# Performance work log

Hardware: AMD Instinct MI355X
Metric: run time of the kernel (lower is better)

The kernel has to match this reference:

```python
import jax, jax.numpy as jnp
import numpy as np

N_NODES = 50000
N_EDGES = 800000
FT = 128
HID = 128
N_EXTRA_LAYERS = 2  # num_layers - 1


def _gin_conv(x, src, dst, W1, b1, W2, b2):
    # GINConv with eps=0: mlp(x + sum_{j->i} x_j)
    agg = jax.ops.segment_sum(x[src], dst, num_segments=N_NODES)
    h = x + agg
    h = jax.nn.relu(h @ W1 + b1)
    return h @ W2 + b2


def setup_inputs() -> dict:
    key = jax.random.key(0)
    ks = jax.random.split(key, 12)
    feat = jax.random.normal(ks[0], (N_NODES, FT), dtype=jnp.float32)
    edge_index = jax.random.randint(ks[1], (2, N_EDGES), 0, N_NODES, dtype=jnp.int32)
    s = 0.02
    # layer 0: ft -> hid
    W1a = jax.random.normal(ks[2], (FT, HID), dtype=jnp.float32) * s
    b1a = jnp.zeros((HID,), dtype=jnp.float32)
    W2a = jax.random.normal(ks[3], (HID, HID), dtype=jnp.float32) * s
    b2a = jnp.zeros((HID,), dtype=jnp.float32)
    # remaining layers stacked: [L, hid, hid]
    Ws1 = jax.random.normal(ks[4], (N_EXTRA_LAYERS, HID, HID), dtype=jnp.float32) * s
    bs1 = jnp.zeros((N_EXTRA_LAYERS, HID), dtype=jnp.float32)
    Ws2 = jax.random.normal(ks[5], (N_EXTRA_LAYERS, HID, HID), dtype=jnp.float32) * s
    bs2 = jnp.zeros((N_EXTRA_LAYERS, HID), dtype=jnp.float32)
    return {"feat": feat, "edge_index": edge_index,
            "W1a": W1a, "b1a": b1a, "W2a": W2a, "b2a": b2a,
            "Ws1": Ws1, "bs1": bs1, "Ws2": Ws2, "bs2": bs2}


def reference(feat, edge_index, W1a, b1a, W2a, b2a, Ws1, bs1, Ws2, bs2):
    src = edge_index[0]
    dst = edge_index[1]
    x = jax.nn.relu(_gin_conv(feat, src, dst, W1a, b1a, W2a, b2a))
    for i in range(N_EXTRA_LAYERS):
        x = jax.nn.relu(_gin_conv(x, src, dst, Ws1[i], bs1[i], Ws2[i], bs2[i]))
    return x[None]  # [1, N, hid]
```

## Files before the change

### kernel.cpp

```cpp
#include <hip/hip_runtime.h>
#include <hip/hip_bf16.h>

#define N_NODES 50000
#define N_EDGES 800000
#define HID 128

typedef __attribute__((ext_vector_type(8))) short bf16x8;
typedef __attribute__((ext_vector_type(4))) float f32x4;

__device__ inline ushort f32_to_bf16_bits(float v) {
    union { float f; unsigned u; } a; a.f = v;
    unsigned r = a.u + 0x7fff + ((a.u >> 16) & 1);
    return (ushort)(r >> 16);
}
__device__ inline float bf16bits_to_f32(ushort b) {
    union { float f; unsigned u; } a; a.u = ((unsigned)b) << 16;
    return a.f;
}


__global__ __launch_bounds__(256) void hist_kernel(const int* __restrict__ dst,
                                                   int* __restrict__ cnt) {
    int e = blockIdx.x * 256 + threadIdx.x;
    if (e < N_EDGES) atomicAdd(&cnt[dst[e]], 1);
}

__global__ __launch_bounds__(256) void alloc_offsets_kernel(const int* __restrict__ cnt,
                                                            int* __restrict__ offs,
                                                            int* __restrict__ cursor,
                                                            int* __restrict__ gcur) {
    int i = blockIdx.x * 256 + threadIdx.x;
    int lane = threadIdx.x & 63;
    int c = (i < N_NODES) ? cnt[i] : 0;
    int pre = c;
    #pragma unroll
    for (int d = 1; d < 64; d <<= 1) {
        int t = __shfl_up(pre, d);
        if (lane >= d) pre += t;
    }
    int base = 0;
    if (lane == 63) base = atomicAdd(gcur, pre);
    base = __shfl(base, 63);
    int o = base + pre - c;
    if (i < N_NODES) { offs[i] = o; cursor[i] = o; }
}

__global__ __launch_bounds__(256) void scatter_kernel(const int* __restrict__ src,
                                                      const int* __restrict__ dst,
                                                      int* __restrict__ cursor,
                                                      int* __restrict__ csr) {
    int e = blockIdx.x * 256 + threadIdx.x;
    if (e < N_EDGES) {
        int d = dst[e];
        int pos = atomicAdd(&cursor[d], 1);
        csr[pos] = src[e];
    }
}


__global__ __launch_bounds__(256) void conv_kernel(const float* __restrict__ in,
                                                   ushort* __restrict__ out) {
    int t = blockIdx.x * 256 + threadIdx.x;
    if (t >= (N_NODES * HID) / 8) return;
    const float4* in4 = (const float4*)in;
    float4 a = in4[2 * t], b = in4[2 * t + 1];
    float v[8] = {a.x, a.y, a.z, a.w, b.x, b.y, b.z, b.w};
    uint4 o;
    o.x = (unsigned)f32_to_bf16_bits(v[0]) | ((unsigned)f32_to_bf16_bits(v[1]) << 16);
    o.y = (unsigned)f32_to_bf16_bits(v[2]) | ((unsigned)f32_to_bf16_bits(v[3]) << 16);
    o.z = (unsigned)f32_to_bf16_bits(v[4]) | ((unsigned)f32_to_bf16_bits(v[5]) << 16);
    o.w = (unsigned)f32_to_bf16_bits(v[6]) | ((unsigned)f32_to_bf16_bits(v[7]) << 16);
    ((uint4*)out)[t] = o;
}


__global__ __launch_bounds__(256) void prep_kernel(const float* __restrict__ W1a,
                                                   const float* __restrict__ W2a,
                                                   const float* __restrict__ Ws1,
                                                   const float* __restrict__ Ws2,
                                                   short* __restrict__ whi,
                                                   short* __restrict__ wlo) {
    int mat = blockIdx.y;
    const float* W;
    switch (mat) {
        case 0: W = W1a; break;
        case 1: W = W2a; break;
        case 2: W = Ws1; break;
        case 3: W = Ws2; break;
        case 4: W = Ws1 + HID * HID; break;
        default: W = Ws2 + HID * HID; break;
    }
    int tid2 = blockIdx.x * 256 + threadIdx.x;
    int l = tid2 & 63;
    int ft = tid2 >> 6;
    int t = ft & 3, f = ft >> 2;
    int g = l >> 4, lm = l & 15;
    bf16x8 hv, lv;
    #pragma unroll
    for (int i = 0; i < 8; ++i) {
        int k = t * 32 + g * 8 + i;
        int n = f * 16 + lm;
        float v = W[k * HID + n];
        ushort hb = f32_to_bf16_bits(v);
        ushort lb = f32_to_bf16_bits(v - bf16bits_to_f32(hb));
        hv[i] = (short)hb;
        lv[i] = (short)lb;
    }
    size_t base = ((size_t)mat * 2048 + tid2) * 8;
    *(bf16x8*)&whi[base] = hv;
    *(bf16x8*)&wlo[base] = lv;
}


__global__ __launch_bounds__(256) void fused_gin_kernel(const unsigned* __restrict__ xbf,
                                                        const int* __restrict__ csr,
                                                        const int* __restrict__ offs,
                                                        const int* __restrict__ cnt,
                                                        const short* __restrict__ w1hi,
                                                        const short* __restrict__ w1lo,
                                                        const short* __restrict__ w2hi,
                                                        const short* __restrict__ w2lo,
                                                        const float* __restrict__ b1,
                                                        const float* __restrict__ b2,
                                                        ushort* __restrict__ xoutb,
                                                        float* __restrict__ xoutf) {
    __shared__ short sHi[16][136];
    __shared__ short sLo[16][136];

    const int tid = threadIdx.x;
    const int lane = tid & 63;
    const int wid = tid >> 6;
    const int nbase = blockIdx.x * 16;
    const int g = lane >> 4, lm = lane & 15;

    for (int n = 0; n < 4; ++n) {
        int node = nbase + wid * 4 + n;
        int off = offs[node];
        int c = cnt[node];
        unsigned su = xbf[(size_t)node * 64 + lane];
        float ax = __uint_as_float(su << 16);
        float ay = __uint_as_float(su & 0xffff0000u);
        int e = 0;
        for (; e + 8 <= c; e += 8) {
            int s[8];
            #pragma unroll
            for (int q = 0; q < 8; ++q) s[q] = csr[off + e + q];
            unsigned u[8];
            #pragma unroll
            for (int q = 0; q < 8; ++q) u[q] = xbf[(size_t)s[q] * 64 + lane];
            #pragma unroll
            for (int q = 0; q < 8; ++q) {
                ax += __uint_as_float(u[q] << 16);
                ay += __uint_as_float(u[q] & 0xffff0000u);
            }
        }
        for (; e + 4 <= c; e += 4) {
            int s0 = csr[off + e], s1 = csr[off + e + 1];
            int s2 = csr[off + e + 2], s3 = csr[off + e + 3];
            unsigned u0 = xbf[(size_t)s0 * 64 + lane];
            unsigned u1 = xbf[(size_t)s1 * 64 + lane];
            unsigned u2 = xbf[(size_t)s2 * 64 + lane];
            unsigned u3 = xbf[(size_t)s3 * 64 + lane];
            ax += (__uint_as_float(u0 << 16) + __uint_as_float(u1 << 16)) +
                  (__uint_as_float(u2 << 16) + __uint_as_float(u3 << 16));
            ay += (__uint_as_float(u0 & 0xffff0000u) + __uint_as_float(u1 & 0xffff0000u)) +
                  (__uint_as_float(u2 & 0xffff0000u) + __uint_as_float(u3 & 0xffff0000u));
        }
        for (; e < c; ++e) {
            int s = csr[off + e];
            unsigned u = xbf[(size_t)s * 64 + lane];
            ax += __uint_as_float(u << 16);
            ay += __uint_as_float(u & 0xffff0000u);
        }
        ushort hx = f32_to_bf16_bits(ax);
        ushort lx = f32_to_bf16_bits(ax - bf16bits_to_f32(hx));
        ushort hy = f32_to_bf16_bits(ay);
        ushort ly = f32_to_bf16_bits(ay - bf16bits_to_f32(hy));
        int row = wid * 4 + n;
        *(unsigned*)&sHi[row][2 * lane] = (unsigned)hx | ((unsigned)hy << 16);
        *(unsigned*)&sLo[row][2 * lane] = (unsigned)lx | ((unsigned)ly << 16);
    }
    __syncthreads();

    f32x4 accT[2];

    {
        bf16x8 ahi[4], alo[4];
        #pragma unroll
        for (int t = 0; t < 4; ++t) {
            ahi[t] = *(bf16x8*)&sHi[lm][t * 32 + g * 8];
            alo[t] = *(bf16x8*)&sLo[lm][t * 32 + g * 8];
        }
        __syncthreads();
        #pragma unroll
        for (int ff = 0; ff < 2; ++ff) {
            int f = wid * 2 + ff;
            const bf16x8* bh = (const bf16x8*)&w1hi[((size_t)(f * 4) * 64 + lane) * 8];
            const bf16x8* bl = (const bf16x8*)&w1lo[((size_t)(f * 4) * 64 + lane) * 8];
            f32x4 acc = {0.f, 0.f, 0.f, 0.f};
            #pragma unroll
            for (int t = 0; t < 4; ++t) {
                bf16x8 bhv = bh[t * 64];
                bf16x8 blv = bl[t * 64];
                acc = __builtin_amdgcn_mfma_f32_16x16x32_bf16(ahi[t], bhv, acc, 0, 0, 0);
                acc = __builtin_amdgcn_mfma_f32_16x16x32_bf16(alo[t], bhv, acc, 0, 0, 0);
                acc = __builtin_amdgcn_mfma_f32_16x16x32_bf16(ahi[t], blv, acc, 0, 0, 0);
            }
            accT[ff] = acc;
        }
    }
    #pragma unroll
    for (int ff = 0; ff < 2; ++ff) {
        int f = wid * 2 + ff;
        float bv = b1[f * 16 + lm];
        #pragma unroll
        for (int r = 0; r < 4; ++r) {
            float v = accT[ff][r] + bv;
            v = v > 0.f ? v : 0.f;
            ushort hb = f32_to_bf16_bits(v);
            ushort lb = f32_to_bf16_bits(v - bf16bits_to_f32(hb));
            int m = g * 4 + r;
            sHi[m][f * 16 + lm] = (short)hb;
            sLo[m][f * 16 + lm] = (short)lb;
        }
    }
    __syncthreads();

    {
        bf16x8 ahi[4], alo[4];
        #pragma unroll
        for (int t = 0; t < 4; ++t) {
            ahi[t] = *(bf16x8*)&sHi[lm][t * 32 + g * 8];
            alo[t] = *(bf16x8*)&sLo[lm][t * 32 + g * 8];
        }
        #pragma unroll
        for (int ff = 0; ff < 2; ++ff) {
            int f = wid * 2 + ff;
            const bf16x8* bh = (const bf16x8*)&w2hi[((size_t)(f * 4) * 64 + lane) * 8];
            const bf16x8* bl = (const bf16x8*)&w2lo[((size_t)(f * 4) * 64 + lane) * 8];
            f32x4 acc = {0.f, 0.f, 0.f, 0.f};
            #pragma unroll
            for (int t = 0; t < 4; ++t) {
                bf16x8 bhv = bh[t * 64];
                bf16x8 blv = bl[t * 64];
                acc = __builtin_amdgcn_mfma_f32_16x16x32_bf16(ahi[t], bhv, acc, 0, 0, 0);
                acc = __builtin_amdgcn_mfma_f32_16x16x32_bf16(alo[t], bhv, acc, 0, 0, 0);
                acc = __builtin_amdgcn_mfma_f32_16x16x32_bf16(ahi[t], blv, acc, 0, 0, 0);
            }
            accT[ff] = acc;
        }
    }
    #pragma unroll
    for (int ff = 0; ff < 2; ++ff) {
        int f = wid * 2 + ff;
        float bv = b2[f * 16 + lm];
        #pragma unroll
        for (int r = 0; r < 4; ++r) {
            float v = accT[ff][r] + bv;
            v = v > 0.f ? v : 0.f;
            int gn = nbase + g * 4 + r;
            size_t gi = (size_t)gn * HID + f * 16 + lm;
            if (xoutb) xoutb[gi] = f32_to_bf16_bits(v);
            if (xoutf) xoutf[gi] = v;
        }
    }
}


extern "C" void kernel_launch(void* const* d_in, const int* in_sizes, int n_in,
                              void* d_out, int out_size, void* d_ws, size_t ws_size,
                              hipStream_t stream) {
    const float* feat = (const float*)d_in[0];
    const int* edge = (const int*)d_in[1];
    const int* src = edge;
    const int* dst = edge + N_EDGES;
    const float* W1a = (const float*)d_in[2];
    const float* b1a = (const float*)d_in[3];
    const float* W2a = (const float*)d_in[4];
    const float* b2a = (const float*)d_in[5];
    const float* Ws1 = (const float*)d_in[6];
    const float* bs1 = (const float*)d_in[7];
    const float* Ws2 = (const float*)d_in[8];
    const float* bs2 = (const float*)d_in[9];
    float* out = (float*)d_out;

    int* cnt = (int*)d_ws;
    int* offs = cnt + 50176;
    int* cursor = offs + 50176;
    int* gcur = cursor + 50176;
    int* csr = gcur + 64;
    ushort* xbA = (ushort*)(csr + N_EDGES);
    ushort* xbB = xbA + (size_t)N_NODES * HID;
    short* whi = (short*)(xbB + (size_t)N_NODES * HID);
    short* wlo = whi + 6 * 2048 * 8;

    hipMemsetAsync(cnt, 0, N_NODES * sizeof(int), stream);
    hipMemsetAsync(gcur, 0, sizeof(int), stream);

    const int EB = (N_EDGES + 255) / 256;
    const int NB = (N_NODES + 255) / 256;
    conv_kernel<<<3125, 256, 0, stream>>>(feat, xbA);
    prep_kernel<<<dim3(8, 6), 256, 0, stream>>>(W1a, W2a, Ws1, Ws2, whi, wlo);
    hist_kernel<<<EB, 256, 0, stream>>>(dst, cnt);
    alloc_offsets_kernel<<<NB, 256, 0, stream>>>(cnt, offs, cursor, gcur);
    scatter_kernel<<<EB, 256, 0, stream>>>(src, dst, cursor, csr);

    const int FB = N_NODES / 16;
    const int MS = 16384;

    fused_gin_kernel<<<FB, 256, 0, stream>>>((const unsigned*)xbA, csr, offs, cnt,
                                             whi + 0 * MS, wlo + 0 * MS,
                                             whi + 1 * MS, wlo + 1 * MS, b1a, b2a,
                                             xbB, nullptr);
    fused_gin_kernel<<<FB, 256, 0, stream>>>((const unsigned*)xbB, csr, offs, cnt,
                                             whi + 2 * MS, wlo + 2 * MS,
                                             whi + 3 * MS, wlo + 3 * MS, bs1, bs2,
                                             xbA, nullptr);
    fused_gin_kernel<<<FB, 256, 0, stream>>>((const unsigned*)xbA, csr, offs, cnt,
                                             whi + 4 * MS, wlo + 4 * MS,
                                             whi + 5 * MS, wlo + 5 * MS,
                                             bs1 + HID, bs2 + HID,
                                             nullptr, out);
}
```

Before: 331.9 us.

## Merge prologue kernels, store CSR indices as 16-bit, unroll gather 16-wide

Combines the feature conversion, weight split and degree histogram into one grid-stride prologue kernel, and folds the two memsets into one. The CSR neighbor list is stored as ushort with nontemporal stores, halving index traffic, and the scatter kernel handles two edges per thread. The gather loop is unrolled to 16 edges to keep more loads in flight. Storing indices in 16 bits truncates node ids, because N_NODES is 50000 and exceeds 65535 only in the sense that any id above 65535 would wrap; here 50000 fits in a ushort, so it is valid only for this node count.

Measured after the change: 337.6 us. No clear change (+1.7%).

```diff
diff --git a/kernel.cpp b/kernel.cpp
--- a/kernel.cpp
+++ b/kernel.cpp
@@ -19,11 +19,68 @@
 }
 
 
-__global__ __launch_bounds__(256) void hist_kernel(const int* __restrict__ dst,
-                                                   int* __restrict__ cnt) {
-    int e = blockIdx.x * 256 + threadIdx.x;
-    if (e < N_EDGES) atomicAdd(&cnt[dst[e]], 1);
-}
+__global__ __launch_bounds__(256) void prologue_kernel(const float* __restrict__ feat,
+                                                       const int* __restrict__ dst,
+                                                       const float* __restrict__ W1a,
+                                                       const float* __restrict__ W2a,
+                                                       const float* __restrict__ Ws1,
+                                                       const float* __restrict__ Ws2,
+                                                       ushort* __restrict__ xbA,
+                                                       short* __restrict__ whi,
+                                                       short* __restrict__ wlo,
+                                                       int* __restrict__ cnt) {
+    const int gtid = blockIdx.x * 256 + threadIdx.x;
+    const int GS = 262144;
+
+    for (int t = gtid; t < 800000; t += GS) {
+        const float4* in4 = (const float4*)feat;
+        float4 a = in4[2 * t], b = in4[2 * t + 1];
+        float v[8] = {a.x, a.y, a.z, a.w, b.x, b.y, b.z, b.w};
+        uint4 o;
+        o.x = (unsigned)f32_to_bf16_bits(v[0]) | ((unsigned)f32_to_bf16_bits(v[1]) << 16);
+        o.y = (unsigned)f32_to_bf16_bits(v[2]) | ((unsigned)f32_to_bf16_bits(v[3]) << 16);
+        o.z = (unsigned)f32_to_bf16_bits(v[4]) | ((unsigned)f32_to_bf16_bits(v[5]) << 16);
+        o.w = (unsigned)f32_to_bf16_bits(v[6]) | ((unsigned)f32_to_bf16_bits(v[7]) << 16);
+        ((uint4*)xbA)[t] = o;
+    }
+
+    if (gtid < 6 * 2048) {
+        int mat = gtid >> 11;
+        int tid2 = gtid & 2047;
+        const float* W;
+        switch (mat) {
+            case 0: W = W1a; break;
+            case 1: W = W2a; break;
+            case 2: W = Ws1; break;
+            case 3: W = Ws2; break;
+            case 4: W = Ws1 + HID * HID; break;
+            default: W = Ws2 + HID * HID; break;
+        }
+        int l = tid2 & 63;
+        int ft = tid2 >> 6;
+        int t = ft & 3, f = ft >> 2;
+        int g = l >> 4, lm = l & 15;
+        bf16x8 hv, lv;
+        #pragma unroll
+        for (int i = 0; i < 8; ++i) {
+            int k = t * 32 + g * 8 + i;
+            int n = f * 16 + lm;
+            float v = W[k * HID + n];
+            ushort hb = f32_to_bf16_bits(v);
+            ushort lb = f32_to_bf16_bits(v - bf16bits_to_f32(hb));
+            hv[i] = (short)hb;
+            lv[i] = (short)lb;
+        }
+        size_t base = ((size_t)mat * 2048 + tid2) * 8;
+        *(bf16x8*)&whi[base] = hv;
+        *(bf16x8*)&wlo[base] = lv;
+    }
+
+    for (int e = gtid; e < N_EDGES; e += GS) {
+        atomicAdd(&cnt[dst[e]], 1);
+    }
+}
+
 
 __global__ __launch_bounds__(256) void alloc_offsets_kernel(const int* __restrict__ cnt,
                                                             int* __restrict__ offs,
@@ -45,75 +102,30 @@
     if (i < N_NODES) { offs[i] = o; cursor[i] = o; }
 }
 
+
 __global__ __launch_bounds__(256) void scatter_kernel(const int* __restrict__ src,
                                                       const int* __restrict__ dst,
                                                       int* __restrict__ cursor,
-                                                      int* __restrict__ csr) {
-    int e = blockIdx.x * 256 + threadIdx.x;
-    if (e < N_EDGES) {
-        int d = dst[e];
-        int pos = atomicAdd(&cursor[d], 1);
-        csr[pos] = src[e];
-    }
-}
-
-
-__global__ __launch_bounds__(256) void conv_kernel(const float* __restrict__ in,
-                                                   ushort* __restrict__ out) {
-    int t = blockIdx.x * 256 + threadIdx.x;
-    if (t >= (N_NODES * HID) / 8) return;
-    const float4* in4 = (const float4*)in;
-    float4 a = in4[2 * t], b = in4[2 * t + 1];
-    float v[8] = {a.x, a.y, a.z, a.w, b.x, b.y, b.z, b.w};
-    uint4 o;
-    o.x = (unsigned)f32_to_bf16_bits(v[0]) | ((unsigned)f32_to_bf16_bits(v[1]) << 16);
-    o.y = (unsigned)f32_to_bf16_bits(v[2]) | ((unsigned)f32_to_bf16_bits(v[3]) << 16);
-    o.z = (unsigned)f32_to_bf16_bits(v[4]) | ((unsigned)f32_to_bf16_bits(v[5]) << 16);
-    o.w = (unsigned)f32_to_bf16_bits(v[6]) | ((unsigned)f32_to_bf16_bits(v[7]) << 16);
-    ((uint4*)out)[t] = o;
-}
-
-
-__global__ __launch_bounds__(256) void prep_kernel(const float* __restrict__ W1a,
-                                                   const float* __restrict__ W2a,
-                                                   const float* __restrict__ Ws1,
-                                                   const float* __restrict__ Ws2,
-                                                   short* __restrict__ whi,
-                                                   short* __restrict__ wlo) {
-    int mat = blockIdx.y;
-    const float* W;
-    switch (mat) {
-        case 0: W = W1a; break;
-        case 1: W = W2a; break;
-        case 2: W = Ws1; break;
-        case 3: W = Ws2; break;
-        case 4: W = Ws1 + HID * HID; break;
-        default: W = Ws2 + HID * HID; break;
-    }
-    int tid2 = blockIdx.x * 256 + threadIdx.x;
-    int l = tid2 & 63;
-    int ft = tid2 >> 6;
-    int t = ft & 3, f = ft >> 2;
-    int g = l >> 4, lm = l & 15;
-    bf16x8 hv, lv;
-    #pragma unroll
-    for (int i = 0; i < 8; ++i) {
-        int k = t * 32 + g * 8 + i;
-        int n = f * 16 + lm;
-        float v = W[k * HID + n];
-        ushort hb = f32_to_bf16_bits(v);
-        ushort lb = f32_to_bf16_bits(v - bf16bits_to_f32(hb));
-        hv[i] = (short)hb;
-        lv[i] = (short)lb;
-    }
-    size_t base = ((size_t)mat * 2048 + tid2) * 8;
-    *(bf16x8*)&whi[base] = hv;
-    *(bf16x8*)&wlo[base] = lv;
+                                                      ushort* __restrict__ csr16) {
+    int e0 = blockIdx.x * 512 + threadIdx.x;
+    int e1 = e0 + 256;
+    int d0 = (e0 < N_EDGES) ? dst[e0] : 0;
+    int d1 = (e1 < N_EDGES) ? dst[e1] : 0;
+    int s0 = (e0 < N_EDGES) ? src[e0] : 0;
+    int s1 = (e1 < N_EDGES) ? src[e1] : 0;
+    if (e0 < N_EDGES) {
+        int p0 = atomicAdd(&cursor[d0], 1);
+        __builtin_nontemporal_store((ushort)s0, &csr16[p0]);
+    }
+    if (e1 < N_EDGES) {
+        int p1 = atomicAdd(&cursor[d1], 1);
+        __builtin_nontemporal_store((ushort)s1, &csr16[p1]);
+    }
 }
 
 
 __global__ __launch_bounds__(256) void fused_gin_kernel(const unsigned* __restrict__ xbf,
-                                                        const int* __restrict__ csr,
+                                                        const ushort* __restrict__ csr16,
                                                         const int* __restrict__ offs,
                                                         const int* __restrict__ cnt,
                                                         const short* __restrict__ w1hi,
@@ -141,22 +153,22 @@
         float ax = __uint_as_float(su << 16);
         float ay = __uint_as_float(su & 0xffff0000u);
         int e = 0;
-        for (; e + 8 <= c; e += 8) {
-            int s[8];
-            #pragma unroll
-            for (int q = 0; q < 8; ++q) s[q] = csr[off + e + q];
-            unsigned u[8];
-            #pragma unroll
-            for (int q = 0; q < 8; ++q) u[q] = xbf[(size_t)s[q] * 64 + lane];
-            #pragma unroll
-            for (int q = 0; q < 8; ++q) {
+        for (; e + 16 <= c; e += 16) {
+            int s[16];
+            #pragma unroll
+            for (int q = 0; q < 16; ++q) s[q] = csr16[off + e + q];
+            unsigned u[16];
+            #pragma unroll
+            for (int q = 0; q < 16; ++q) u[q] = xbf[(size_t)s[q] * 64 + lane];
+            #pragma unroll
+            for (int q = 0; q < 16; ++q) {
                 ax += __uint_as_float(u[q] << 16);
                 ay += __uint_as_float(u[q] & 0xffff0000u);
             }
         }
         for (; e + 4 <= c; e += 4) {
-            int s0 = csr[off + e], s1 = csr[off + e + 1];
-            int s2 = csr[off + e + 2], s3 = csr[off + e + 3];
+            int s0 = csr16[off + e], s1 = csr16[off + e + 1];
+            int s2 = csr16[off + e + 2], s3 = csr16[off + e + 3];
             unsigned u0 = xbf[(size_t)s0 * 64 + lane];
             unsigned u1 = xbf[(size_t)s1 * 64 + lane];
             unsigned u2 = xbf[(size_t)s2 * 64 + lane];
@@ -167,7 +179,7 @@
                   (__uint_as_float(u2 & 0xffff0000u) + __uint_as_float(u3 & 0xffff0000u));
         }
         for (; e < c; ++e) {
-            int s = csr[off + e];
+            int s = csr16[off + e];
             unsigned u = xbf[(size_t)s * 64 + lane];
             ax += __uint_as_float(u << 16);
             ay += __uint_as_float(u & 0xffff0000u);
@@ -285,38 +297,34 @@
     float* out = (float*)d_out;
 
     int* cnt = (int*)d_ws;
-    int* offs = cnt + 50176;
+    int* gcur = cnt + 50176;
+    int* offs = gcur + 64;
     int* cursor = offs + 50176;
-    int* gcur = cursor + 50176;
-    int* csr = gcur + 64;
-    ushort* xbA = (ushort*)(csr + N_EDGES);
+    ushort* csr16 = (ushort*)(cursor + 50176);
+    ushort* xbA = csr16 + N_EDGES;
     ushort* xbB = xbA + (size_t)N_NODES * HID;
     short* whi = (short*)(xbB + (size_t)N_NODES * HID);
     short* wlo = whi + 6 * 2048 * 8;
 
-    hipMemsetAsync(cnt, 0, N_NODES * sizeof(int), stream);
-    hipMemsetAsync(gcur, 0, sizeof(int), stream);
-
-    const int EB = (N_EDGES + 255) / 256;
-    const int NB = (N_NODES + 255) / 256;
-    conv_kernel<<<3125, 256, 0, stream>>>(feat, xbA);
-    prep_kernel<<<dim3(8, 6), 256, 0, stream>>>(W1a, W2a, Ws1, Ws2, whi, wlo);
-    hist_kernel<<<EB, 256, 0, stream>>>(dst, cnt);
-    alloc_offsets_kernel<<<NB, 256, 0, stream>>>(cnt, offs, cursor, gcur);
-    scatter_kernel<<<EB, 256, 0, stream>>>(src, dst, cursor, csr);
+    hipMemsetAsync(cnt, 0, (50176 + 64) * sizeof(int), stream);
+
+    prologue_kernel<<<1024, 256, 0, stream>>>(feat, dst, W1a, W2a, Ws1, Ws2,
+                                              xbA, whi, wlo, cnt);
+    alloc_offsets_kernel<<<(N_NODES + 255) / 256, 256, 0, stream>>>(cnt, offs, cursor, gcur);
+    scatter_kernel<<<(N_EDGES + 511) / 512, 256, 0, stream>>>(src, dst, cursor, csr16);
 
     const int FB = N_NODES / 16;
     const int MS = 16384;
 
-    fused_gin_kernel<<<FB, 256, 0, stream>>>((const unsigned*)xbA, csr, offs, cnt,
+    fused_gin_kernel<<<FB, 256, 0, stream>>>((const unsigned*)xbA, csr16, offs, cnt,
                                              whi + 0 * MS, wlo + 0 * MS,
                                              whi + 1 * MS, wlo + 1 * MS, b1a, b2a,
                                              xbB, nullptr);
-    fused_gin_kernel<<<FB, 256, 0, stream>>>((const unsigned*)xbB, csr, offs, cnt,
+    fused_gin_kernel<<<FB, 256, 0, stream>>>((const unsigned*)xbB, csr16, offs, cnt,
                                              whi + 2 * MS, wlo + 2 * MS,
                                              whi + 3 * MS, wlo + 3 * MS, bs1, bs2,
                                              xbA, nullptr);
-    fused_gin_kernel<<<FB, 256, 0, stream>>>((const unsigned*)xbA, csr, offs, cnt,
+    fused_gin_kernel<<<FB, 256, 0, stream>>>((const unsigned*)xbA, csr16, offs, cnt,
                                              whi + 4 * MS, wlo + 4 * MS,
                                              whi + 5 * MS, wlo + 5 * MS,
                                              bs1 + HID, bs2 + HID,
```
